# Kernel optimization log

Hardware: AMD Instinct MI355X
Metric: run time of the kernel (lower is better)

## Reference

```python
import jax, jax.numpy as jnp
import numpy as np

D_G = 16384; B = 128; NNZ = 262144
CL1_F = 32; CL1_K = 6; FC1_F = 512; FC2_F = 512
NN_FC1 = 512; NN_FC2 = 256
CL4_F = 32; CL4_K = 4; FC1_G4 = 128; FC2_G4 = 64
OUT = 10; POOL1 = 8; POOL4 = 3; V4 = 10; EMB = 64
FC1FIN = CL1_F * (D_G // POOL1)        # 65536
G4OUT = CL4_F * (OUT // POOL4)         # 96
SUMFIN = FC1_F + NN_FC2 + FC2_G4 + 64  # 896


def _cheby(x, W, b, spmm, K):
    # x: [B, V, Fin]; Chebyshev recursion T_k(L) x with K-order feature stacking
    Bb, V, Fin = x.shape
    x0 = jnp.transpose(x, (1, 2, 0)).reshape(V, Fin * Bb)
    xs = [x0]
    if K > 1:
        x1 = spmm(x0)
        xs.append(x1)
        for _ in range(K - 2):
            x2 = 2.0 * spmm(x1) - x0
            xs.append(x2)
            x0, x1 = x1, x2
    X = jnp.stack(xs).reshape(K, V, Fin, Bb)
    X = jnp.transpose(X, (3, 1, 2, 0)).reshape(Bb * V, Fin * K)  # [B*V, Fin*K]
    return (X @ W.T + b).reshape(Bb, V, -1)


def _gmaxpool(x, p):
    # MaxPool1d(p) over node dim (floor truncation like torch)
    Bb, V, F = x.shape
    Vp = (V // p) * p
    return x[:, :Vp].reshape(Bb, V // p, p, F).max(axis=2)


def setup_inputs():
    key = jax.random.key(0)
    ks = jax.random.split(key, 32)
    def lin(i, fo, fi):
        return (jax.random.normal(ks[i], (fo, fi), jnp.float32) * 0.02,
                jnp.zeros((fo,), jnp.float32))
    cl1_W, cl1_b = lin(0, CL1_F, CL1_K)
    fc1_W, fc1_b = lin(1, FC1_F, FC1FIN)
    fc2_W, fc2_b = lin(2, FC2_F, FC1_F)
    fc3_W, fc3_b = lin(3, D_G, FC2_F)
    nn1_W, nn1_b = lin(4, NN_FC1, D_G)
    nn2_W, nn2_b = lin(5, NN_FC2, NN_FC1)
    cl4_W, cl4_b = lin(6, CL4_F, CL4_K * EMB)
    fcg1_W, fcg1_b = lin(7, FC1_G4, G4OUT)
    fcg2_W, fcg2_b = lin(8, FC2_G4, FC1_G4)
    nn14_W, nn14_b = lin(9, 256, V4 * EMB)
    nn24_W, nn24_b = lin(10, 64, 256)
    fcsum_W, fcsum_b = lin(11, OUT, SUMFIN)
    return {
        'x_in': jax.random.normal(ks[12], (B, D_G), jnp.float32),
        'x_embed': jax.random.normal(ks[13], (V4, EMB), jnp.float32),
        'dropout': 0,
        'L_rows': jnp.sort(jax.random.randint(ks[14], (NNZ,), 0, D_G)),
        'L_cols': jax.random.randint(ks[15], (NNZ,), 0, D_G),
        'L_vals': jax.random.normal(ks[16], (NNZ,), jnp.float32) * 0.1,
        'L_mg': jax.random.normal(ks[17], (V4, V4), jnp.float32) * 0.2,
        'cl1_W': cl1_W, 'cl1_b': cl1_b, 'fc1_W': fc1_W, 'fc1_b': fc1_b,
        'fc2_W': fc2_W, 'fc2_b': fc2_b, 'fc3_W': fc3_W, 'fc3_b': fc3_b,
        'nn1_W': nn1_W, 'nn1_b': nn1_b, 'nn2_W': nn2_W, 'nn2_b': nn2_b,
        'cl4_W': cl4_W, 'cl4_b': cl4_b, 'fcg1_W': fcg1_W, 'fcg1_b': fcg1_b,
        'fcg2_W': fcg2_W, 'fcg2_b': fcg2_b, 'nn14_W': nn14_W, 'nn14_b': nn14_b,
        'nn24_W': nn24_W, 'nn24_b': nn24_b, 'fcsum_W': fcsum_W, 'fcsum_b': fcsum_b,
    }


def reference(x_in, x_embed, dropout, L_rows, L_cols, L_vals, L_mg,
              cl1_W, cl1_b, fc1_W, fc1_b, fc2_W, fc2_b, fc3_W, fc3_b,
              nn1_W, nn1_b, nn2_W, nn2_b, cl4_W, cl4_b,
              fcg1_W, fcg1_b, fcg2_W, fcg2_b, nn14_W, nn14_b, nn24_W, nn24_b,
              fcsum_W, fcsum_b):
    Bb = x_in.shape[0]
    def spmm_L(m):  # COO SpMM: y[r] += v * m[c]
        return jax.ops.segment_sum(L_vals[:, None] * m[L_cols], L_rows,
                                   num_segments=D_G)
    # --- GCN 1 (gene graph) ---
    x = _cheby(x_in[:, :, None], cl1_W, cl1_b, spmm_L, CL1_K)
    x = jax.nn.relu(x)
    x = _gmaxpool(x, POOL1).reshape(Bb, FC1FIN)
    x_hidden_gae = jax.nn.relu(x @ fc1_W.T + fc1_b)
    # FC2_F != 0 branch; dropout p=0 is identity at this baseline
    x_decode_gae = jax.nn.relu(x_hidden_gae @ fc2_W.T + fc2_b)
    x_decode_gae = x_decode_gae @ fc3_W.T + fc3_b
    # --- NN 1 ---
    x_nn = jax.nn.relu(x_in @ nn1_W.T + nn1_b)
    x_nn = jax.nn.relu(x_nn @ nn2_W.T + nn2_b)
    # --- GCN 4 (small meta-graph, dense Laplacian) ---
    xe = jnp.broadcast_to(x_embed[None], (Bb, V4, EMB))
    xg = _cheby(xe, cl4_W, cl4_b, lambda m: L_mg @ m, CL4_K)
    xg = jax.nn.relu(xg)
    xg = _gmaxpool(xg, POOL4).reshape(Bb, G4OUT)
    xg = jax.nn.relu(xg @ fcg1_W.T + fcg1_b)
    xg = jax.nn.relu(xg @ fcg2_W.T + fcg2_b)
    # --- NN of GCN4 ---
    xn4 = xe.reshape(Bb, V4 * EMB)
    xn4 = jax.nn.relu(xn4 @ nn14_W.T + nn14_b)
    xn4 = jax.nn.relu(xn4 @ nn24_W.T + nn24_b)
    data_emb = jnp.concatenate([x_hidden_gae, x_nn, xg, xn4], axis=1)
    logp = jax.nn.log_softmax(data_emb @ fcsum_W.T + fcsum_b, axis=-1)
    return x_decode_gae, x_hidden_gae, logp
```

## Files before the change

kernel.cpp:

```cpp
#include <hip/hip_runtime.h>
#include <hip/hip_bf16.h>

#define DG 16384
#define NNZ 262144
#define BB 128

typedef __attribute__((ext_vector_type(8))) short bf16x8;
typedef __attribute__((ext_vector_type(8))) unsigned short us8;
typedef __attribute__((ext_vector_type(4))) float f32x4;
typedef __attribute__((ext_vector_type(4))) unsigned short us4;
typedef __attribute__((ext_vector_type(2))) float f32x2;

#define WS_ROWPTR 0
#define WS_XIN16  66048
#define WS_T      4260352
#define WS_XPOOL  54592000
#define WS_XB0    71369216
#define WS_XB1    75563520
#define WS_XNN1B  79757824
#define WS_DEC2   79888896
#define WS_XNN2   80019968
#define WS_HIDB   80151040
#define WS_N1     80282112
#define WS_TAIL   80283136
#define WS_PNN1   81000448
#define WS_PFC1   97777664

__device__ __forceinline__ unsigned short f2bf(float f) {
  __hip_bfloat16 h = __float2bfloat16(f);
  return __builtin_bit_cast(unsigned short, h);
}
__device__ __forceinline__ float bflo(unsigned u) {
  return __builtin_bit_cast(float, u << 16);
}
__device__ __forceinline__ float bfhi(unsigned u) {
  return __builtin_bit_cast(float, u & 0xffff0000u);
}

__device__ void prep_dev(const float* __restrict__ x_in, const int* __restrict__ rows,
                         int* __restrict__ rowptr, unsigned short* __restrict__ xin16,
                         int bid) {
  int idx = bid * 256 + threadIdx.x;
  if (idx <= DG) {
    int lo = 0, hi = NNZ;
    while (lo < hi) { int mid = (lo + hi) >> 1; if (rows[mid] < idx) lo = mid + 1; else hi = mid; }
    rowptr[idx] = lo;
  }
  f32x4 v = ((const f32x4*)x_in)[idx];
  us4 o; o[0] = f2bf(v[0]); o[1] = f2bf(v[1]); o[2] = f2bf(v[2]); o[3] = f2bf(v[3]);
  ((us4*)xin16)[idx] = o;
}

__device__ void transpose_dev(const float* __restrict__ x_in, float* __restrict__ T0,
                              unsigned short* __restrict__ Xb0, int id) {
  __shared__ float tl[32][33];
  int bx = id & 511, by = id >> 9;
  int v0 = bx * 32, b0 = by * 32;
  int tx = threadIdx.x & 31, ty0 = threadIdx.x >> 5;
  #pragma unroll
  for (int j = 0; j < 4; ++j) {
    int ty = ty0 + j * 8;
    tl[ty][tx] = x_in[(size_t)(b0 + ty) * DG + v0 + tx];
  }
  __syncthreads();
  #pragma unroll
  for (int j = 0; j < 4; ++j) {
    int ty = ty0 + j * 8;
    float v = tl[tx][ty];
    size_t o = (size_t)(v0 + ty) * BB + b0 + tx;
    T0[o] = v;
    Xb0[o] = f2bf(v);
  }
}

__device__ void dot4_dev(const float* __restrict__ x, const float* __restrict__ W,
                         const float* __restrict__ bias, float* __restrict__ out,
                         int K, int id) {
  int w = threadIdx.x >> 6, lane = threadIdx.x & 63;
  int o = id * 4 + w;
  float a = 0.f;
  for (int i = lane; i < K; i += 64) a += x[i] * W[(size_t)o * K + i];
  #pragma unroll
  for (int s = 32; s > 0; s >>= 1) a += __shfl_down(a, s);
  if (lane == 0) out[o] = fmaxf(a + bias[o], 0.f);
}

__device__ void g4_dev(const float* __restrict__ xe_g, const float* __restrict__ Lmg_g,
                       const float* __restrict__ W4, const float* __restrict__ b4,
                       const float* __restrict__ Wg1, const float* __restrict__ bg1,
                       const float* __restrict__ Wg2, const float* __restrict__ bg2,
                       float* __restrict__ tail) {
  __shared__ float Lm[100], Tg[4][640], xc[320], xg96[96], h1[128];
  int t = threadIdx.x;
  for (int i = t; i < 640; i += 256) Tg[0][i] = xe_g[i];
  for (int i = t; i < 100; i += 256) Lm[i] = Lmg_g[i];
  __syncthreads();
  for (int i = t; i < 640; i += 256) {
    int v = i >> 6, f = i & 63; float s = 0.f;
    #pragma unroll
    for (int u = 0; u < 10; ++u) s += Lm[v * 10 + u] * Tg[0][u * 64 + f];
    Tg[1][i] = s;
  }
  __syncthreads();
  for (int kk = 2; kk < 4; ++kk) {
    for (int i = t; i < 640; i += 256) {
      int v = i >> 6, f = i & 63; float s = 0.f;
      #pragma unroll
      for (int u = 0; u < 10; ++u) s += Lm[v * 10 + u] * Tg[kk - 1][u * 64 + f];
      Tg[kk][i] = 2.f * s - Tg[kk - 2][i];
    }
    __syncthreads();
  }
  for (int i = t; i < 320; i += 256) {
    int v = i >> 5, fo = i & 31; float s = b4[fo];
    for (int fin = 0; fin < 64; ++fin)
      #pragma unroll
      for (int k = 0; k < 4; ++k) s += Tg[k][v * 64 + fin] * W4[fo * 256 + fin * 4 + k];
    xc[i] = fmaxf(s, 0.f);
  }
  __syncthreads();
  for (int i = t; i < 96; i += 256) {
    int g = i >> 5, fo = i & 31;
    xg96[i] = fmaxf(fmaxf(xc[(3 * g) * 32 + fo], xc[(3 * g + 1) * 32 + fo]),
                    xc[(3 * g + 2) * 32 + fo]);
  }
  __syncthreads();
  for (int o = t; o < 128; o += 256) {
    float s = bg1[o];
    for (int i2 = 0; i2 < 96; ++i2) s += xg96[i2] * Wg1[o * 96 + i2];
    h1[o] = fmaxf(s, 0.f);
  }
  __syncthreads();
  for (int o = t; o < 64; o += 256) {
    float s = bg2[o];
    for (int i2 = 0; i2 < 128; ++i2) s += h1[i2] * Wg2[o * 128 + i2];
    tail[o] = fmaxf(s, 0.f);
  }
}

__global__ __launch_bounds__(256) void setup_kernel(
    const float* __restrict__ x_in, const int* __restrict__ rows,
    int* __restrict__ rowptr, unsigned short* __restrict__ xin16,
    float* __restrict__ T0, unsigned short* __restrict__ Xb0,
    const float* __restrict__ x_embed,
    const float* __restrict__ nn14_W, const float* __restrict__ nn14_b,
    float* __restrict__ n1,
    const float* __restrict__ Lmg, const float* __restrict__ W4,
    const float* __restrict__ b4, const float* __restrict__ Wg1,
    const float* __restrict__ bg1, const float* __restrict__ Wg2,
    const float* __restrict__ bg2, float* __restrict__ tail) {
  int bid = blockIdx.x;
  if (bid < 1) g4_dev(x_embed, Lmg, W4, b4, Wg1, bg1, Wg2, bg2, tail);
  else if (bid < 65) dot4_dev(x_embed, nn14_W, nn14_b, n1, 640, bid - 1);
  else if (bid < 2113) prep_dev(x_in, rows, rowptr, xin16, bid - 65);
  else transpose_dev(x_in, T0, Xb0, bid - 2113);
}

__global__ __launch_bounds__(256) void spmm3(
    const int* __restrict__ rowptr, const int* __restrict__ cols,
    const float* __restrict__ vals, const unsigned* __restrict__ X2,
    const float* __restrict__ Tprev, float* __restrict__ Tout,
    unsigned* __restrict__ Xbout, float scale) {
  int r = blockIdx.x * 4 + (threadIdx.x >> 6);
  int lane = threadIdx.x & 63;
  int e0 = rowptr[r], e1 = rowptr[r + 1];
  float a00 = 0.f, a01 = 0.f, a10 = 0.f, a11 = 0.f;
  int e = e0;
  for (; e + 4 <= e1; e += 4) {
    int c0 = cols[e], c1 = cols[e + 1], c2 = cols[e + 2], c3 = cols[e + 3];
    float v0 = vals[e], v1 = vals[e + 1], v2 = vals[e + 2], v3 = vals[e + 3];
    unsigned x0 = X2[c0 * 64 + lane], x1 = X2[c1 * 64 + lane];
    unsigned x2 = X2[c2 * 64 + lane], x3 = X2[c3 * 64 + lane];
    a00 += v0 * bflo(x0); a10 += v0 * bfhi(x0);
    a01 += v1 * bflo(x1); a11 += v1 * bfhi(x1);
    a00 += v2 * bflo(x2); a10 += v2 * bfhi(x2);
    a01 += v3 * bflo(x3); a11 += v3 * bfhi(x3);
  }
  for (; e < e1; ++e) {
    float v = vals[e]; unsigned x = X2[cols[e] * 64 + lane];
    a00 += v * bflo(x); a10 += v * bfhi(x);
  }
  float s0 = scale * (a00 + a01), s1 = scale * (a10 + a11);
  size_t o = (size_t)r * BB + lane * 2;
  if (Tprev) { f32x2 p = *(const f32x2*)(Tprev + o); s0 -= p[0]; s1 -= p[1]; }
  *(f32x2*)(Tout + o) = (f32x2){s0, s1};
  Xbout[(size_t)r * 64 + lane] = (unsigned)f2bf(s0) | ((unsigned)f2bf(s1) << 16);
}

__device__ void combine_dev(const float* __restrict__ Tbase, const float* __restrict__ W,
                            const float* __restrict__ bias, unsigned short* __restrict__ xpool,
                            int vp) {
  __shared__ float tile[6][8][128];
  __shared__ float Wl[192];
  __shared__ float bl[32];
  for (int i = threadIdx.x; i < 192; i += 256) Wl[i] = W[i];
  if (threadIdx.x < 32) bl[threadIdx.x] = bias[threadIdx.x];
  for (int i = threadIdx.x; i < 6144; i += 256) {
    int k = i >> 10, rem = i & 1023, j = rem >> 7, b = rem & 127;
    tile[k][j][b] = Tbase[(size_t)k * 2097152 + (size_t)(vp * 8 + j) * BB + b];
  }
  __syncthreads();
  for (int p = threadIdx.x; p < 4096; p += 256) {
    int b = p >> 5, f = p & 31;
    float m = -1e30f;
    #pragma unroll
    for (int j = 0; j < 8; ++j) {
      float s = bl[f];
      #pragma unroll
      for (int k = 0; k < 6; ++k) s += tile[k][j][b] * Wl[f * 6 + k];
      m = fmaxf(m, s);
    }
    m = fmaxf(m, 0.f);
    xpool[(size_t)b * 65536 + vp * 32 + f] = f2bf(m);
  }
}

__global__ __launch_bounds__(256) void combine_nn24(
    const float* __restrict__ Tbase, const float* __restrict__ W,
    const float* __restrict__ bias, unsigned short* __restrict__ xpool,
    const float* __restrict__ n1, const float* __restrict__ nn24_W,
    const float* __restrict__ nn24_b, float* __restrict__ tail64) {
  int bid = blockIdx.x;
  if (bid < 2048) combine_dev(Tbase, W, bias, xpool, bid);
  else dot4_dev(n1, nn24_W, nn24_b, tail64, 256, bid - 2048);
}

template<int NT, int MT>
__device__ void gemm_core4(
    unsigned short* __restrict__ Alds,
    unsigned short* __restrict__ Wlds,
    const unsigned short* __restrict__ A, const float* __restrict__ W,
    float* __restrict__ outP, unsigned short* __restrict__ outB,
    const float* __restrict__ bias, int K, int N, int Kchunk,
    int bx, int by, int row0, int relu, int partial) {
  const int LA = MT / 2;
  const int LW = NT * 4;
  int t = threadIdx.x, w = t >> 6, lane = t & 63, lr = lane & 15, lg = lane >> 4;
  int n0 = bx * NT * 64;
  int kbeg = by * Kchunk;
  f32x4 acc[MT][NT];
  #pragma unroll
  for (int mt = 0; mt < MT; ++mt)
    #pragma unroll
    for (int nt = 0; nt < NT; ++nt) acc[mt][nt] = (f32x4){0.f, 0.f, 0.f, 0.f};
  int rowA[LA], kkA[LA], rowW[LW], kkW[LW];
  #pragma unroll
  for (int j = 0; j < LA; ++j) { int idx = j * 256 + t; rowA[j] = idx >> 3; kkA[j] = (idx & 7) * 8; }
  #pragma unroll
  for (int j = 0; j < LW; ++j) { int idx = j * 256 + t; rowW[j] = idx >> 4; kkW[j] = (idx & 15) * 4; }
  int stages = Kchunk >> 6;
  for (int s = 0; s < stages; ++s) {
    int k0 = kbeg + s * 64;
    __syncthreads();
    #pragma unroll
    for (int j = 0; j < LA; ++j) {
      us8 v = *(const us8*)(A + (size_t)(row0 + rowA[j]) * K + k0 + kkA[j]);
      *(us8*)(Alds + rowA[j] * 64 + (kkA[j] ^ ((rowA[j] & 7) << 3))) = v;
    }
    #pragma unroll
    for (int j = 0; j < LW; ++j) {
      f32x4 v = *(const f32x4*)(W + (size_t)(n0 + rowW[j]) * K + k0 + kkW[j]);
      us4 o; o[0] = f2bf(v[0]); o[1] = f2bf(v[1]); o[2] = f2bf(v[2]); o[3] = f2bf(v[3]);
      *(us4*)(Wlds + rowW[j] * 64 + (kkW[j] ^ ((rowW[j] & 7) << 3))) = o;
    }
    __syncthreads();
    #pragma unroll
    for (int h = 0; h < 2; ++h) {
      int k32 = h * 32;
      bf16x8 bfr[NT];
      #pragma unroll
      for (int nt = 0; nt < NT; ++nt) {
        int wrow = w * NT * 16 + nt * 16 + lr;
        bfr[nt] = *(const bf16x8*)(Wlds + wrow * 64 + ((k32 + lg * 8) ^ ((wrow & 7) << 3)));
      }
      #pragma unroll
      for (int mt = 0; mt < MT; ++mt) {
        int arow = mt * 16 + lr;
        bf16x8 af = *(const bf16x8*)(Alds + arow * 64 + ((k32 + lg * 8) ^ ((arow & 7) << 3)));
        #pragma unroll
        for (int nt = 0; nt < NT; ++nt)
          acc[mt][nt] = __builtin_amdgcn_mfma_f32_16x16x32_bf16(af, bfr[nt], acc[mt][nt], 0, 0, 0);
      }
    }
  }
  if (partial) {
    float* P = outP + (size_t)by * 128 * (size_t)N;
    #pragma unroll
    for (int mt = 0; mt < MT; ++mt)
      #pragma unroll
      for (int nt = 0; nt < NT; ++nt) {
        int col = n0 + w * NT * 16 + nt * 16 + lr;
        #pragma unroll
        for (int r2 = 0; r2 < 4; ++r2) {
          int row = row0 + mt * 16 + lg * 4 + r2;
          P[(size_t)row * N + col] = acc[mt][nt][r2];
        }
      }
  } else {
    #pragma unroll
    for (int mt = 0; mt < MT; ++mt)
      #pragma unroll
      for (int nt = 0; nt < NT; ++nt) {
        int col = n0 + w * NT * 16 + nt * 16 + lr;
        float bc = bias[col];
        #pragma unroll
        for (int r2 = 0; r2 < 4; ++r2) {
          int row = row0 + mt * 16 + lg * 4 + r2;
          float v = acc[mt][nt][r2] + bc;
          if (relu) v = fmaxf(v, 0.f);
          if (outP) outP[(size_t)row * N + col] = v;
          if (outB) outB[(size_t)row * N + col] = f2bf(v);
        }
      }
  }
}

__global__ __launch_bounds__(256) void gemm_partials(
    const unsigned short* __restrict__ xin16, const float* __restrict__ nn1_W,
    const unsigned short* __restrict__ xpool, const float* __restrict__ fc1_W,
    float* __restrict__ pnn1, float* __restrict__ pfc1) {
  __shared__ unsigned short Alds[128 * 64];
  __shared__ unsigned short Wlds[128 * 64];
  int nb = blockIdx.x;
  if (nb < 256) {
    int xcd = nb & 7, q = nb >> 3, bx = q & 3, by = ((q >> 2) << 3) | xcd;
    gemm_core4<2, 8>(Alds, Wlds, xin16, nn1_W, pnn1, nullptr, nullptr,
                     16384, 512, 256, bx, by, 0, 0, 1);
  } else {
    int b = nb - 256;
    int xcd = b & 7, q = b >> 3, bx = q & 3, by = ((q >> 2) << 3) | xcd;
    gemm_core4<2, 8>(Alds, Wlds, xpool, fc1_W, pfc1, nullptr, nullptr,
                     65536, 512, 256, bx, by, 0, 0, 1);
  }
}

__global__ __launch_bounds__(256) void reduce_fused(
    const float* __restrict__ pfc1, const float* __restrict__ fc1_b,
    float* __restrict__ hidden, unsigned short* __restrict__ hidB,
    const float* __restrict__ pnn1, const float* __restrict__ nn1_b,
    unsigned short* __restrict__ xnn1b) {
  int b = blockIdx.x;
  if (b < 256) {
    int idx = b * 256 + threadIdx.x;
    float s = 0.f;
    for (int i = 0; i < 256; ++i) s += pfc1[(size_t)i * 65536 + idx];
    float v = fmaxf(s + fc1_b[idx & 511], 0.f);
    hidden[idx] = v;
    hidB[idx] = f2bf(v);
  } else {
    int idx = (b - 256) * 256 + threadIdx.x;
    float s = 0.f;
    for (int i = 0; i < 64; ++i) s += pnn1[(size_t)i * 65536 + idx];
    float v = fmaxf(s + nn1_b[idx & 511], 0.f);
    xnn1b[idx] = f2bf(v);
  }
}

__global__ __launch_bounds__(256) void fc2nn2_kernel(
    const unsigned short* __restrict__ hidB, const float* __restrict__ fc2_W,
    const float* __restrict__ fc2_b, unsigned short* __restrict__ dec2,
    const unsigned short* __restrict__ xnn1b, const float* __restrict__ nn2_W,
    const float* __restrict__ nn2_b, float* __restrict__ xnn2) {
  __shared__ unsigned short Alds[128 * 64];
  __shared__ unsigned short Wlds[64 * 64];
  int b = blockIdx.x;
  if (b < 8)
    gemm_core4<1, 8>(Alds, Wlds, hidB, fc2_W, nullptr, dec2, fc2_b,
                     512, 512, 512, b, 0, 0, 1, 0);
  else
    gemm_core4<1, 8>(Alds, Wlds, xnn1b, nn2_W, xnn2, nullptr, nn2_b,
                     512, 256, 512, b - 8, 0, 0, 1, 0);
}

__device__ void fcsum_dev(int id, const float* __restrict__ hidden,
                          const float* __restrict__ xnn2, const float* __restrict__ tail,
                          const float* __restrict__ Ws, const float* __restrict__ bs,
                          float* __restrict__ logp) {
  __shared__ float emb[4][896];
  int w = threadIdx.x >> 6, lane = threadIdx.x & 63;
  int b = id * 4 + w;
  for (int i = lane; i < 896; i += 64)
    emb[w][i] = (i < 512) ? hidden[b * 512 + i]
              : (i < 768) ? xnn2[b * 256 + (i - 512)]
                          : tail[i - 768];
  __syncthreads();
  float l[10];
  #pragma unroll
  for (int o = 0; o < 10; ++o) {
    float a = 0.f;
    for (int i = lane; i < 896; i += 64) a += emb[w][i] * Ws[o * 896 + i];
    #pragma unroll
    for (int s = 32; s > 0; s >>= 1) a += __shfl_down(a, s);
    l[o] = __shfl(a, 0) + bs[o];
  }
  float m = l[0];
  #pragma unroll
  for (int o = 1; o < 10; ++o) m = fmaxf(m, l[o]);
  float sum = 0.f;
  #pragma unroll
  for (int o = 0; o < 10; ++o) sum += expf(l[o] - m);
  float lse = m + logf(sum);
  #pragma unroll
  for (int o = 0; o < 10; ++o)
    if (lane == o) logp[b * 10 + o] = l[o] - lse;
}

__global__ __launch_bounds__(256) void fc3_head(
    const unsigned short* __restrict__ dec2, const float* __restrict__ fc3_W,
    const float* __restrict__ fc3_b, float* __restrict__ out0,
    const float* __restrict__ hidden, const float* __restrict__ xnn2,
    const float* __restrict__ tail, const float* __restrict__ fcsum_W,
    const float* __restrict__ fcsum_b, float* __restrict__ logp) {
  __shared__ unsigned short Alds[64 * 64];
  __shared__ unsigned short Wlds[64 * 64];
  int b = blockIdx.x;
  if (b < 1024) {
    int bx = b >> 2, my = b & 3;
    gemm_core4<1, 2>(Alds, Wlds, dec2, fc3_W, out0, nullptr, fc3_b,
                     512, 16384, 512, bx, 0, my * 32, 0, 0);
  } else {
    fcsum_dev(b - 1024, hidden, xnn2, tail, fcsum_W, fcsum_b, logp);
  }
}

extern "C" void kernel_launch(void* const* d_in, const int* in_sizes, int n_in,
                              void* d_out, int out_size, void* d_ws, size_t ws_size,
                              hipStream_t stream) {
  const float* x_in    = (const float*)d_in[0];
  const float* x_embed = (const float*)d_in[1];
  const int*   L_rows  = (const int*)d_in[3];
  const int*   L_cols  = (const int*)d_in[4];
  const float* L_vals  = (const float*)d_in[5];
  const float* L_mg    = (const float*)d_in[6];
  const float* cl1_W = (const float*)d_in[7],  *cl1_b = (const float*)d_in[8];
  const float* fc1_W = (const float*)d_in[9],  *fc1_b = (const float*)d_in[10];
  const float* fc2_W = (const float*)d_in[11], *fc2_b = (const float*)d_in[12];
  const float* fc3_W = (const float*)d_in[13], *fc3_b = (const float*)d_in[14];
  const float* nn1_W = (const float*)d_in[15], *nn1_b = (const float*)d_in[16];
  const float* nn2_W = (const float*)d_in[17], *nn2_b = (const float*)d_in[18];
  const float* cl4_W = (const float*)d_in[19], *cl4_b = (const float*)d_in[20];
  const float* fcg1_W = (const float*)d_in[21], *fcg1_b = (const float*)d_in[22];
  const float* fcg2_W = (const float*)d_in[23], *fcg2_b = (const float*)d_in[24];
  const float* nn14_W = (const float*)d_in[25], *nn14_b = (const float*)d_in[26];
  const float* nn24_W = (const float*)d_in[27], *nn24_b = (const float*)d_in[28];
  const float* fcsum_W = (const float*)d_in[29], *fcsum_b = (const float*)d_in[30];

  char* ws = (char*)d_ws;
  int* rowptr = (int*)(ws + WS_ROWPTR);
  unsigned short* xin16 = (unsigned short*)(ws + WS_XIN16);
  float* T = (float*)(ws + WS_T);
  unsigned short* xpool = (unsigned short*)(ws + WS_XPOOL);
  unsigned short* Xb0 = (unsigned short*)(ws + WS_XB0);
  unsigned short* Xb1 = (unsigned short*)(ws + WS_XB1);
  unsigned short* xnn1b = (unsigned short*)(ws + WS_XNN1B);
  unsigned short* dec2 = (unsigned short*)(ws + WS_DEC2);
  float* xnn2 = (float*)(ws + WS_XNN2);
  unsigned short* hidB = (unsigned short*)(ws + WS_HIDB);
  float* n1 = (float*)(ws + WS_N1);
  float* tail = (float*)(ws + WS_TAIL);
  float* pnn1 = (float*)(ws + WS_PNN1);
  float* pfc1 = (float*)(ws + WS_PFC1);

  float* out0 = (float*)d_out;
  float* hidden = out0 + 2097152;
  float* logp = out0 + 2097152 + 65536;

  setup_kernel<<<4161, 256, 0, stream>>>(x_in, L_rows, rowptr, xin16, T, Xb0,
                                         x_embed, nn14_W, nn14_b, n1,
                                         L_mg, cl4_W, cl4_b, fcg1_W, fcg1_b,
                                         fcg2_W, fcg2_b, tail);

  spmm3<<<4096, 256, 0, stream>>>(rowptr, L_cols, L_vals, (const unsigned*)Xb0,
                                  nullptr,          T + 1 * 2097152, (unsigned*)Xb1, 1.f);
  spmm3<<<4096, 256, 0, stream>>>(rowptr, L_cols, L_vals, (const unsigned*)Xb1,
                                  T,                T + 2 * 2097152, (unsigned*)Xb0, 2.f);
  spmm3<<<4096, 256, 0, stream>>>(rowptr, L_cols, L_vals, (const unsigned*)Xb0,
                                  T + 1 * 2097152,  T + 3 * 2097152, (unsigned*)Xb1, 2.f);
  spmm3<<<4096, 256, 0, stream>>>(rowptr, L_cols, L_vals, (const unsigned*)Xb1,
                                  T + 2 * 2097152,  T + 4 * 2097152, (unsigned*)Xb0, 2.f);
  spmm3<<<4096, 256, 0, stream>>>(rowptr, L_cols, L_vals, (const unsigned*)Xb0,
                                  T + 3 * 2097152,  T + 5 * 2097152, (unsigned*)Xb1, 2.f);

  combine_nn24<<<2064, 256, 0, stream>>>(T, cl1_W, cl1_b, xpool,
                                         n1, nn24_W, nn24_b, tail + 64);

  gemm_partials<<<1280, 256, 0, stream>>>(xin16, nn1_W, xpool, fc1_W, pnn1, pfc1);

  reduce_fused<<<512, 256, 0, stream>>>(pfc1, fc1_b, hidden, hidB,
                                        pnn1, nn1_b, xnn1b);

  fc2nn2_kernel<<<12, 256, 0, stream>>>(hidB, fc2_W, fc2_b, dec2,
                                        xnn1b, nn2_W, nn2_b, xnn2);

  fc3_head<<<1056, 256, 0, stream>>>(dec2, fc3_W, fc3_b, out0,
                                     hidden, xnn2, tail, fcsum_W, fcsum_b, logp);
}
```

Before: 317.1 us.

## Load GEMM weights straight into registers, bypassing LDS, and halve split-K partials

The GEMM core now has each lane load its own fp32 weight fragment with nontemporal loads, converting it to bf16 in registers instead of staging it through LDS. This removes the W shared-memory buffer and its conversion and store traffic. Split-K chunk size doubles for the fc1 and nn1 partial GEMMs, which halves the partial buffers the reduction kernel must read. fc3 tiles grow to 64 rows, and occupancy hints are added. Risks are uncoalesced per-lane weight loads, fewer blocks in flight, and higher register pressure.

```diff
diff --git a/kernel.cpp b/kernel.cpp
--- a/kernel.cpp
+++ b/kernel.cpp
@@ -35,6 +35,9 @@
 }
 __device__ __forceinline__ float bfhi(unsigned u) {
   return __builtin_bit_cast(float, u & 0xffff0000u);
+}
+__device__ __forceinline__ f32x4 ntload4(const float* p) {
+  return __builtin_nontemporal_load((const f32x4*)p);
 }
 
 __device__ void prep_dev(const float* __restrict__ x_in, const int* __restrict__ rows,
@@ -226,15 +229,13 @@
 }
 
 template<int NT, int MT>
-__device__ void gemm_core4(
+__device__ void gemm_core5(
     unsigned short* __restrict__ Alds,
-    unsigned short* __restrict__ Wlds,
     const unsigned short* __restrict__ A, const float* __restrict__ W,
     float* __restrict__ outP, unsigned short* __restrict__ outB,
     const float* __restrict__ bias, int K, int N, int Kchunk,
     int bx, int by, int row0, int relu, int partial) {
   const int LA = MT / 2;
-  const int LW = NT * 4;
   int t = threadIdx.x, w = t >> 6, lane = t & 63, lr = lane & 15, lg = lane >> 4;
   int n0 = bx * NT * 64;
   int kbeg = by * Kchunk;
@@ -243,25 +244,24 @@
   for (int mt = 0; mt < MT; ++mt)
     #pragma unroll
     for (int nt = 0; nt < NT; ++nt) acc[mt][nt] = (f32x4){0.f, 0.f, 0.f, 0.f};
-  int rowA[LA], kkA[LA], rowW[LW], kkW[LW];
-  #pragma unroll
-  for (int j = 0; j < LA; ++j) { int idx = j * 256 + t; rowA[j] = idx >> 3; kkA[j] = (idx & 7) * 8; }
-  #pragma unroll
-  for (int j = 0; j < LW; ++j) { int idx = j * 256 + t; rowW[j] = idx >> 4; kkW[j] = (idx & 15) * 4; }
+  const float* Wbase = W + (size_t)(n0 + w * NT * 16 + lr) * K + lg * 8;
   int stages = Kchunk >> 6;
   for (int s = 0; s < stages; ++s) {
     int k0 = kbeg + s * 64;
+    f32x4 rw[NT][4];
+    #pragma unroll
+    for (int nt = 0; nt < NT; ++nt) {
+      const float* wp = Wbase + (size_t)nt * 16 * K + k0;
+      rw[nt][0] = ntload4(wp);      rw[nt][1] = ntload4(wp + 4);
+      rw[nt][2] = ntload4(wp + 32); rw[nt][3] = ntload4(wp + 36);
+    }
     __syncthreads();
     #pragma unroll
     for (int j = 0; j < LA; ++j) {
-      us8 v = *(const us8*)(A + (size_t)(row0 + rowA[j]) * K + k0 + kkA[j]);
-      *(us8*)(Alds + rowA[j] * 64 + (kkA[j] ^ ((rowA[j] & 7) << 3))) = v;
-    }
-    #pragma unroll
-    for (int j = 0; j < LW; ++j) {
-      f32x4 v = *(const f32x4*)(W + (size_t)(n0 + rowW[j]) * K + k0 + kkW[j]);
-      us4 o; o[0] = f2bf(v[0]); o[1] = f2bf(v[1]); o[2] = f2bf(v[2]); o[3] = f2bf(v[3]);
-      *(us4*)(Wlds + rowW[j] * 64 + (kkW[j] ^ ((rowW[j] & 7) << 3))) = o;
+      int idx = j * 256 + t;
+      int row = idx >> 3, kk = (idx & 7) * 8;
+      us8 v = *(const us8*)(A + (size_t)(row0 + row) * K + k0 + kk);
+      *(us8*)(Alds + row * 64 + (kk ^ ((row & 7) << 3))) = v;
     }
     __syncthreads();
     #pragma unroll
@@ -270,8 +270,13 @@
       bf16x8 bfr[NT];
       #pragma unroll
       for (int nt = 0; nt < NT; ++nt) {
-        int wrow = w * NT * 16 + nt * 16 + lr;
-        bfr[nt] = *(const bf16x8*)(Wlds + wrow * 64 + ((k32 + lg * 8) ^ ((wrow & 7) << 3)));
+        f32x4 w0 = rw[nt][h * 2], w1 = rw[nt][h * 2 + 1];
+        bf16x8 bv;
+        bv[0] = (short)f2bf(w0[0]); bv[1] = (short)f2bf(w0[1]);
+        bv[2] = (short)f2bf(w0[2]); bv[3] = (short)f2bf(w0[3]);
+        bv[4] = (short)f2bf(w1[0]); bv[5] = (short)f2bf(w1[1]);
+        bv[6] = (short)f2bf(w1[2]); bv[7] = (short)f2bf(w1[3]);
+        bfr[nt] = bv;
       }
       #pragma unroll
       for (int mt = 0; mt < MT; ++mt) {
@@ -315,22 +320,21 @@
   }
 }
 
-__global__ __launch_bounds__(256) void gemm_partials(
+__global__ __launch_bounds__(256, 4) void gemm_partials(
     const unsigned short* __restrict__ xin16, const float* __restrict__ nn1_W,
     const unsigned short* __restrict__ xpool, const float* __restrict__ fc1_W,
     float* __restrict__ pnn1, float* __restrict__ pfc1) {
   __shared__ unsigned short Alds[128 * 64];
-  __shared__ unsigned short Wlds[128 * 64];
   int nb = blockIdx.x;
-  if (nb < 256) {
+  if (nb < 128) {
     int xcd = nb & 7, q = nb >> 3, bx = q & 3, by = ((q >> 2) << 3) | xcd;
-    gemm_core4<2, 8>(Alds, Wlds, xin16, nn1_W, pnn1, nullptr, nullptr,
-                     16384, 512, 256, bx, by, 0, 0, 1);
+    gemm_core5<2, 8>(Alds, xin16, nn1_W, pnn1, nullptr, nullptr,
+                     16384, 512, 512, bx, by, 0, 0, 1);
   } else {
-    int b = nb - 256;
+    int b = nb - 128;
     int xcd = b & 7, q = b >> 3, bx = q & 3, by = ((q >> 2) << 3) | xcd;
-    gemm_core4<2, 8>(Alds, Wlds, xpool, fc1_W, pfc1, nullptr, nullptr,
-                     65536, 512, 256, bx, by, 0, 0, 1);
+    gemm_core5<2, 8>(Alds, xpool, fc1_W, pfc1, nullptr, nullptr,
+                     65536, 512, 512, bx, by, 0, 0, 1);
   }
 }
 
@@ -343,32 +347,31 @@
   if (b < 256) {
     int idx = b * 256 + threadIdx.x;
     float s = 0.f;
-    for (int i = 0; i < 256; ++i) s += pfc1[(size_t)i * 65536 + idx];
+    for (int i = 0; i < 128; ++i) s += pfc1[(size_t)i * 65536 + idx];
     float v = fmaxf(s + fc1_b[idx & 511], 0.f);
     hidden[idx] = v;
     hidB[idx] = f2bf(v);
   } else {
     int idx = (b - 256) * 256 + threadIdx.x;
     float s = 0.f;
-    for (int i = 0; i < 64; ++i) s += pnn1[(size_t)i * 65536 + idx];
+    for (int i = 0; i < 32; ++i) s += pnn1[(size_t)i * 65536 + idx];
     float v = fmaxf(s + nn1_b[idx & 511], 0.f);
     xnn1b[idx] = f2bf(v);
   }
 }
 
-__global__ __launch_bounds__(256) void fc2nn2_kernel(
+__global__ __launch_bounds__(256, 4) void fc2nn2_kernel(
     const unsigned short* __restrict__ hidB, const float* __restrict__ fc2_W,
     const float* __restrict__ fc2_b, unsigned short* __restrict__ dec2,
     const unsigned short* __restrict__ xnn1b, const float* __restrict__ nn2_W,
     const float* __restrict__ nn2_b, float* __restrict__ xnn2) {
   __shared__ unsigned short Alds[128 * 64];
-  __shared__ unsigned short Wlds[64 * 64];
   int b = blockIdx.x;
   if (b < 8)
-    gemm_core4<1, 8>(Alds, Wlds, hidB, fc2_W, nullptr, dec2, fc2_b,
+    gemm_core5<1, 8>(Alds, hidB, fc2_W, nullptr, dec2, fc2_b,
                      512, 512, 512, b, 0, 0, 1, 0);
   else
-    gemm_core4<1, 8>(Alds, Wlds, xnn1b, nn2_W, xnn2, nullptr, nn2_b,
+    gemm_core5<1, 8>(Alds, xnn1b, nn2_W, xnn2, nullptr, nn2_b,
                      512, 256, 512, b - 8, 0, 0, 1, 0);
 }
 
@@ -405,21 +408,20 @@
     if (lane == o) logp[b * 10 + o] = l[o] - lse;
 }
 
-__global__ __launch_bounds__(256) void fc3_head(
+__global__ __launch_bounds__(256, 4) void fc3_head(
     const unsigned short* __restrict__ dec2, const float* __restrict__ fc3_W,
     const float* __restrict__ fc3_b, float* __restrict__ out0,
     const float* __restrict__ hidden, const float* __restrict__ xnn2,
     const float* __restrict__ tail, const float* __restrict__ fcsum_W,
     const float* __restrict__ fcsum_b, float* __restrict__ logp) {
   __shared__ unsigned short Alds[64 * 64];
-  __shared__ unsigned short Wlds[64 * 64];
   int b = blockIdx.x;
-  if (b < 1024) {
-    int bx = b >> 2, my = b & 3;
-    gemm_core4<1, 2>(Alds, Wlds, dec2, fc3_W, out0, nullptr, fc3_b,
-                     512, 16384, 512, bx, 0, my * 32, 0, 0);
+  if (b < 512) {
+    int bx = b >> 1, my = b & 1;
+    gemm_core5<1, 4>(Alds, dec2, fc3_W, out0, nullptr, fc3_b,
+                     512, 16384, 512, bx, 0, my * 64, 0, 0);
   } else {
-    fcsum_dev(b - 1024, hidden, xnn2, tail, fcsum_W, fcsum_b, logp);
+    fcsum_dev(b - 512, hidden, xnn2, tail, fcsum_W, fcsum_b, logp);
   }
 }
 
@@ -484,7 +486,7 @@
   combine_nn24<<<2064, 256, 0, stream>>>(T, cl1_W, cl1_b, xpool,
                                          n1, nn24_W, nn24_b, tail + 64);
 
-  gemm_partials<<<1280, 256, 0, stream>>>(xin16, nn1_W, xpool, fc1_W, pnn1, pfc1);
+  gemm_partials<<<640, 256, 0, stream>>>(xin16, nn1_W, xpool, fc1_W, pnn1, pfc1);
 
   reduce_fused<<<512, 256, 0, stream>>>(pfc1, fc1_b, hidden, hidB,
                                         pnn1, nn1_b, xnn1b);
@@ -492,6 +494,6 @@
   fc2nn2_kernel<<<12, 256, 0, stream>>>(hidB, fc2_W, fc2_b, dec2,
                                         xnn1b, nn2_W, nn2_b, xnn2);
 
-  fc3_head<<<1056, 256, 0, stream>>>(dec2, fc3_W, fc3_b, out0,
-                                     hidden, xnn2, tail, fcsum_W, fcsum_b, logp);
-}
+  fc3_head<<<544, 256, 0, stream>>>(dec2, fc3_W, fc3_b, out0,
+                                    hidden, xnn2, tail, fcsum_W, fcsum_b, logp);
+}
```

Result: faster. 284.9 us (-10.2%).
